# Kernel tuning notes

Hardware: AMD Instinct MI355X
Metric: run time of the kernel (lower is better)

## Reference

```python
import jax, jax.numpy as jnp
import numpy as np

N = 50000      # nodes
E = 800000     # edges (avg degree 16)
IN = 128       # in_dim0
H = 96         # hidden_dim
BN_EPS = 1e-5
PN_SCALE = 20.0


def setup_inputs() -> dict:
    key = jax.random.key(0)
    ks = jax.random.split(key, 12)
    s_in = 1.0 / np.sqrt(IN)
    s_h = 1.0 / np.sqrt(H)
    return {
        "x": jax.random.normal(ks[0], (N, IN), jnp.float32),
        "edge_index": jax.random.randint(ks[1], (2, E), 0, N, jnp.int32),
        # mlp0: Linear(in_dim0 -> hidden)
        "W0": jax.random.uniform(ks[2], (H, IN), jnp.float32, -s_in, s_in),
        "b0": jax.random.uniform(ks[3], (H,), jnp.float32, -s_in, s_in),
        # GIN MLP layer 1: Linear(hidden -> hidden) + BatchNorm
        "W1": jax.random.uniform(ks[4], (H, H), jnp.float32, -s_h, s_h),
        "b1": jax.random.uniform(ks[5], (H,), jnp.float32, -s_h, s_h),
        "gamma": jnp.ones((H,), jnp.float32),
        "beta": jnp.zeros((H,), jnp.float32),
        # GIN MLP layer 2: Linear(hidden -> hidden)
        "W2": jax.random.uniform(ks[6], (H, H), jnp.float32, -s_h, s_h),
        "b2": jax.random.uniform(ks[7], (H,), jnp.float32, -s_h, s_h),
    }


def reference(x, edge_index, W0, b0, W1, b1, gamma, beta, W2, b2):
    # h0 = mlp0(x)
    h0 = x @ W0.T + b0                                   # [N, H]

    # GINConv (eps=0): z_i = h0_i + sum_{j->i} h0_j
    src, dst = edge_index[0], edge_index[1]
    agg = jax.ops.segment_sum(h0[src], dst, num_segments=N)  # [N, H]
    z = h0 + agg

    # GIN MLP (layer_num=2): Linear -> BatchNorm(train) -> ReLU -> Linear
    h = z @ W1.T + b1
    mean = h.mean(axis=0)
    var = h.var(axis=0)                                  # biased, like torch BN
    h = (h - mean) * jax.lax.rsqrt(var + BN_EPS) * gamma + beta
    h = jax.nn.relu(h)
    l1 = h @ W2.T + b2                                   # [N, H]

    # PairNorm 'PN-SCS', scale=20
    col_mean = l1.mean(axis=0)
    rownorm = jnp.sqrt(1e-6 + jnp.sum(l1 * l1, axis=1, keepdims=True))
    l1 = PN_SCALE * l1 / rownorm - col_mean

    return (l1, h0)
```

## Files before the change

### kernel.cpp

```cpp
#include <hip/hip_runtime.h>

#define NN 50000
#define IN_DIM 128
#define HD 96
#define BN_EPS 1e-5f
#define PN_SCALE 20.0f
#define SCAN_NB 196

__device__ __forceinline__ float4 ld4(const float* p) { return *(const float4*)p; }
__device__ __forceinline__ float4 add4(float4 a, float4 b) {
    return make_float4(a.x + b.x, a.y + b.y, a.z + b.z, a.w + b.w);
}

__global__ void zero_kernel(float* stats, int* cnt) {
    int i = blockIdx.x * blockDim.x + threadIdx.x;
    if (i < 1024) stats[i] = 0.0f;
    int j = i - 1024;
    if (j >= 0 && j < NN) cnt[j] = 0;
}

template<int K, int MODE>
__global__ __launch_bounds__(256) void gemm_tiled(
    const float* A, const float* __restrict__ W, const float* __restrict__ bias,
    float* out, const float* __restrict__ scale, const float* __restrict__ shift,
    float* __restrict__ gsum, float* __restrict__ gsumsq,
    float* __restrict__ gcol, float* __restrict__ growss,
    const int* __restrict__ hist_dst, int* __restrict__ hist_cnt, int histE)
{
    constexpr int CK = 32;
    __shared__ float sh[64 * (CK + 1) + HD * (CK + 1)];
    float* As = sh;
    float* Ws = sh + 64 * (CK + 1);

    const int t  = threadIdx.x;

    if (MODE == 0) {
        int e0 = blockIdx.x * 1024 + t * 4;
#pragma unroll
        for (int i = 0; i < 4; ++i) {
            int e = e0 + i;
            if (e < histE) atomicAdd(&hist_cnt[hist_dst[e]], 1);
        }
    }

    const int tx = t & 15;
    const int ty = t >> 4;
    const int base = blockIdx.x * 64;

    float acc[4][6];
#pragma unroll
    for (int i = 0; i < 4; ++i)
#pragma unroll
        for (int j = 0; j < 6; ++j) acc[i][j] = 0.0f;

    for (int kc = 0; kc < K; kc += CK) {
#pragma unroll
        for (int it = 0; it < 2; ++it) {
            int q = t + it * 256;
            int r = q >> 3, c4 = q & 7;
            int row = base + r;
            float4 v = make_float4(0.f, 0.f, 0.f, 0.f);
            if (row < NN) v = ld4(A + (size_t)row * K + kc + c4 * 4);
            if (MODE == 2) {
                float4 sc = ld4(scale + kc + c4 * 4);
                float4 shf = ld4(shift + kc + c4 * 4);
                v.x = fmaxf(v.x * sc.x + shf.x, 0.f);
                v.y = fmaxf(v.y * sc.y + shf.y, 0.f);
                v.z = fmaxf(v.z * sc.z + shf.z, 0.f);
                v.w = fmaxf(v.w * sc.w + shf.w, 0.f);
            }
            float* d = As + r * (CK + 1) + c4 * 4;
            d[0] = v.x; d[1] = v.y; d[2] = v.z; d[3] = v.w;
        }
#pragma unroll
        for (int it = 0; it < 3; ++it) {
            int q = t + it * 256;
            int r = q >> 3, c4 = q & 7;
            float4 v = ld4(W + (size_t)r * K + kc + c4 * 4);
            float* d = Ws + r * (CK + 1) + c4 * 4;
            d[0] = v.x; d[1] = v.y; d[2] = v.z; d[3] = v.w;
        }
        __syncthreads();
#pragma unroll
        for (int kk = 0; kk < CK; ++kk) {
            float a[4], b[6];
#pragma unroll
            for (int i = 0; i < 4; ++i) a[i] = As[(ty * 4 + i) * (CK + 1) + kk];
#pragma unroll
            for (int j = 0; j < 6; ++j) b[j] = Ws[(tx * 6 + j) * (CK + 1) + kk];
#pragma unroll
            for (int i = 0; i < 4; ++i)
#pragma unroll
                for (int j = 0; j < 6; ++j) acc[i][j] += a[i] * b[j];
        }
        __syncthreads();
    }

    float cv[4][6];
#pragma unroll
    for (int j = 0; j < 6; ++j) {
        float bs = bias[tx * 6 + j];
#pragma unroll
        for (int i = 0; i < 4; ++i) cv[i][j] = acc[i][j] + bs;
    }
#pragma unroll
    for (int i = 0; i < 4; ++i) {
        int row = base + ty * 4 + i;
        if (row < NN) {
#pragma unroll
            for (int j = 0; j < 6; ++j)
                out[(size_t)row * HD + tx * 6 + j] = cv[i][j];
        }
    }

    if (MODE == 1) {
        float* rs_sum = sh;
        float* rs_sq  = sh + 1536;
        __syncthreads();
#pragma unroll
        for (int j = 0; j < 6; ++j) {
            float s = 0.f, q = 0.f;
#pragma unroll
            for (int i = 0; i < 4; ++i) {
                int row = base + ty * 4 + i;
                float v = (row < NN) ? cv[i][j] : 0.f;
                s += v; q += v * v;
            }
            rs_sum[ty * HD + tx * 6 + j] = s;
            rs_sq[ty * HD + tx * 6 + j]  = q;
        }
        __syncthreads();
        if (t < HD) {
            float S = 0.f, Q = 0.f;
#pragma unroll
            for (int r = 0; r < 16; ++r) { S += rs_sum[r * HD + t]; Q += rs_sq[r * HD + t]; }
            atomicAdd(&gsum[t], S);
            atomicAdd(&gsumsq[t], Q);
        }
    }

    if (MODE == 2) {
        float* rs_sum = sh;
        float* rr     = sh + 1536;
        __syncthreads();
#pragma unroll
        for (int j = 0; j < 6; ++j) {
            float s = 0.f;
#pragma unroll
            for (int i = 0; i < 4; ++i) {
                int row = base + ty * 4 + i;
                s += (row < NN) ? cv[i][j] : 0.f;
            }
            rs_sum[ty * HD + tx * 6 + j] = s;
        }
#pragma unroll
        for (int i = 0; i < 4; ++i) {
            float q = 0.f;
#pragma unroll
            for (int j = 0; j < 6; ++j) q += cv[i][j] * cv[i][j];
            rr[(ty * 4 + i) * 16 + tx] = q;
        }
        __syncthreads();
        if (t < HD) {
            float S = 0.f;
#pragma unroll
            for (int r = 0; r < 16; ++r) S += rs_sum[r * HD + t];
            atomicAdd(&gcol[t], S);
        }
        if (t < 64) {
            int row = base + t;
            if (row < NN) {
                float S = 0.f;
#pragma unroll
                for (int g = 0; g < 16; ++g) S += rr[t * 16 + g];
                growss[row] = S;
            }
        }
    }
}

__global__ __launch_bounds__(256) void scan_part1(const int* __restrict__ cnt,
                                                  int* __restrict__ bsum) {
    __shared__ int sh[256];
    int i = blockIdx.x * 256 + threadIdx.x;
    int t = threadIdx.x;
    sh[t] = (i < NN) ? cnt[i] : 0;
    __syncthreads();
    for (int off = 128; off > 0; off >>= 1) {
        if (t < off) sh[t] += sh[t + off];
        __syncthreads();
    }
    if (t == 0) bsum[blockIdx.x] = sh[0];
}

__global__ __launch_bounds__(256) void scan_part2(int* __restrict__ bsum) {
    __shared__ int sh[256];
    int t = threadIdx.x;
    int v = (t < SCAN_NB) ? bsum[t] : 0;
    sh[t] = v;
    __syncthreads();
    for (int off = 1; off < 256; off <<= 1) {
        int u = sh[t];
        if (t >= off) u += sh[t - off];
        __syncthreads();
        sh[t] = u;
        __syncthreads();
    }
    if (t < SCAN_NB) bsum[t] = sh[t] - v;
}

__global__ __launch_bounds__(256) void scan_part3(int* __restrict__ cnt,
                                                  const int* __restrict__ bsum,
                                                  int* __restrict__ rowptr) {
    __shared__ int sh[256];
    int i = blockIdx.x * 256 + threadIdx.x;
    int t = threadIdx.x;
    int v = (i < NN) ? cnt[i] : 0;
    sh[t] = v;
    __syncthreads();
    for (int off = 1; off < 256; off <<= 1) {
        int u = sh[t];
        if (t >= off) u += sh[t - off];
        __syncthreads();
        sh[t] = u;
        __syncthreads();
    }
    int excl = sh[t] - v + bsum[blockIdx.x];
    if (i < NN) { rowptr[i] = excl; cnt[i] = excl; }
    if (i == NN - 1) rowptr[NN] = excl + v;
}

__global__ __launch_bounds__(256) void fill_kernel(const int* __restrict__ ei,
                                                   int* __restrict__ cursor,
                                                   int* __restrict__ srcs, int E) {
    int t2 = blockIdx.x * 256 + threadIdx.x;
    int e0 = t2 * 2;
    int src[2], dst[2];
#pragma unroll
    for (int i = 0; i < 2; ++i) {
        int e = e0 + i;
        bool ok = e < E;
        dst[i] = ok ? ei[E + e] : -1;
        src[i] = ok ? ei[e] : 0;
    }
    for (int pass = 0; pass < 7; ++pass) {
#pragma unroll
        for (int i = 0; i < 2; ++i) {
            if (dst[i] >= 0 && (dst[i] >> 13) == pass) {
                int slot = atomicAdd(&cursor[dst[i]], 1);
                srcs[slot] = src[i];
            }
        }
    }
}

__global__ __launch_bounds__(192) void gather_kernel(
    const float* __restrict__ h0, const int* __restrict__ rowptr,
    const int* __restrict__ srcs, float* __restrict__ z)
{
    const int tid = threadIdx.x;
    const int rl  = tid / 24;
    const int c   = tid - rl * 24;
    const int row = blockIdx.x * 8 + rl;
    if (row >= NN) return;

    const int p0 = rowptr[row];
    const int p1 = rowptr[row + 1];

    float4 acc = ld4(h0 + (size_t)row * HD + c * 4);

    int p = p0;
    for (; p + 8 <= p1; p += 8) {
        int s0 = srcs[p + 0], s1 = srcs[p + 1], s2 = srcs[p + 2], s3 = srcs[p + 3];
        int s4 = srcs[p + 4], s5 = srcs[p + 5], s6 = srcs[p + 6], s7 = srcs[p + 7];
        float4 v0 = ld4(h0 + (size_t)s0 * HD + c * 4);
        float4 v1 = ld4(h0 + (size_t)s1 * HD + c * 4);
        float4 v2 = ld4(h0 + (size_t)s2 * HD + c * 4);
        float4 v3 = ld4(h0 + (size_t)s3 * HD + c * 4);
        float4 v4 = ld4(h0 + (size_t)s4 * HD + c * 4);
        float4 v5 = ld4(h0 + (size_t)s5 * HD + c * 4);
        float4 v6 = ld4(h0 + (size_t)s6 * HD + c * 4);
        float4 v7 = ld4(h0 + (size_t)s7 * HD + c * 4);
        acc = add4(acc, add4(add4(add4(v0, v1), add4(v2, v3)),
                             add4(add4(v4, v5), add4(v6, v7))));
    }
    for (; p + 4 <= p1; p += 4) {
        int s0 = srcs[p + 0], s1 = srcs[p + 1], s2 = srcs[p + 2], s3 = srcs[p + 3];
        float4 v0 = ld4(h0 + (size_t)s0 * HD + c * 4);
        float4 v1 = ld4(h0 + (size_t)s1 * HD + c * 4);
        float4 v2 = ld4(h0 + (size_t)s2 * HD + c * 4);
        float4 v3 = ld4(h0 + (size_t)s3 * HD + c * 4);
        acc = add4(acc, add4(add4(v0, v1), add4(v2, v3)));
    }
    for (; p < p1; ++p)
        acc = add4(acc, ld4(h0 + (size_t)srcs[p] * HD + c * 4));

    *(float4*)(z + (size_t)row * HD + c * 4) = acc;
}

__global__ void bn_finalize_kernel(const float* __restrict__ sum, const float* __restrict__ sumsq,
                                   const float* __restrict__ gamma, const float* __restrict__ beta,
                                   float* __restrict__ scale, float* __restrict__ shift)
{
    int f = threadIdx.x;
    if (f < HD) {
        float mean = sum[f] * (1.0f / NN);
        float var  = fmaxf(sumsq[f] * (1.0f / NN) - mean * mean, 0.0f);
        float rstd = rsqrtf(var + BN_EPS);
        float sc = rstd * gamma[f];
        scale[f] = sc;
        shift[f] = beta[f] - mean * sc;
    }
}

__global__ __launch_bounds__(256) void pn_kernel(float* l1, const float* __restrict__ colsum,
                                                 const float* __restrict__ rowss)
{
    int idx = blockIdx.x * 256 + threadIdx.x;
    if (idx >= NN * 24) return;
    int row = idx / 24;
    int q = idx - row * 24;
    float rs = rsqrtf(1e-6f + rowss[row]);
    float4 v = ld4(l1 + (size_t)idx * 4);
    float4 cm = ld4(colsum + q * 4);
    v.x = PN_SCALE * v.x * rs - cm.x * (1.0f / NN);
    v.y = PN_SCALE * v.y * rs - cm.y * (1.0f / NN);
    v.z = PN_SCALE * v.z * rs - cm.z * (1.0f / NN);
    v.w = PN_SCALE * v.w * rs - cm.w * (1.0f / NN);
    *(float4*)(l1 + (size_t)idx * 4) = v;
}

extern "C" void kernel_launch(void* const* d_in, const int* in_sizes, int n_in,
                              void* d_out, int out_size, void* d_ws, size_t ws_size,
                              hipStream_t stream) {
    const float* x     = (const float*)d_in[0];
    const int*   ei    = (const int*)d_in[1];
    const float* W0    = (const float*)d_in[2];
    const float* b0    = (const float*)d_in[3];
    const float* W1    = (const float*)d_in[4];
    const float* b1    = (const float*)d_in[5];
    const float* gamma = (const float*)d_in[6];
    const float* beta  = (const float*)d_in[7];
    const float* W2    = (const float*)d_in[8];
    const float* b2    = (const float*)d_in[9];

    float* out_l1 = (float*)d_out;
    float* out_h0 = out_l1 + (size_t)NN * HD;

    float* stats   = (float*)d_ws;
    float* s_sum   = stats;
    float* s_sumsq = stats + HD;
    float* s_col   = stats + 2 * HD;
    float* s_scale = stats + 288;
    float* s_shift = stats + 384;
    float* rowss = stats + 1024;
    int* cnt    = (int*)(rowss + NN);
    int* rowptr = cnt + NN;
    int* bsum   = rowptr + NN + 2;
    int* srcs   = bsum + 256;

    const int E = in_sizes[1] / 2;
    const int GB = (NN + 63) / 64;

    zero_kernel<<<(1024 + NN + 255) / 256, 256, 0, stream>>>(stats, cnt);
    gemm_tiled<IN_DIM, 0><<<GB, 256, 0, stream>>>(x, W0, b0, out_h0, nullptr, nullptr,
                                                  nullptr, nullptr, nullptr, nullptr,
                                                  ei + E, cnt, E);
    scan_part1<<<SCAN_NB, 256, 0, stream>>>(cnt, bsum);
    scan_part2<<<1, 256, 0, stream>>>(bsum);
    scan_part3<<<SCAN_NB, 256, 0, stream>>>(cnt, bsum, rowptr);
    fill_kernel<<<(E / 2 + 255) / 256, 256, 0, stream>>>(ei, cnt, srcs, E);
    gather_kernel<<<(NN + 7) / 8, 192, 0, stream>>>(out_h0, rowptr, srcs, out_l1);
    gemm_tiled<HD, 1><<<GB, 256, 0, stream>>>(out_l1, W1, b1, out_l1, nullptr, nullptr,
                                              s_sum, s_sumsq, nullptr, nullptr,
                                              nullptr, nullptr, 0);
    bn_finalize_kernel<<<1, 128, 0, stream>>>(s_sum, s_sumsq, gamma, beta, s_scale, s_shift);
    gemm_tiled<HD, 2><<<GB, 256, 0, stream>>>(out_l1, W2, b2, out_l1, s_scale, s_shift,
                                              nullptr, nullptr, s_col, rowss,
                                              nullptr, nullptr, 0);
    pn_kernel<<<(NN * 24 + 255) / 256, 256, 0, stream>>>(out_l1, s_col, rowss);
}
```

Baseline: 337.6 us.

## Restructure GEMM tiles: transposed smem, vectorized reads, register prefetch

Changes the per-thread tile from 4x6 to 2x12 and stores A and W transposed in shared memory with padding, so the inner loop uses float2/float4 LDS reads instead of scalar ones. Global loads for the next K chunk are prefetched into registers while the current chunk computes (software pipelining). Output stores and bias loads are vectorized, and the BN/PairNorm reductions are adapted to the new 32x8 thread layout. This aims to cut LDS instruction count and hide global latency, at the cost of more registers and transposed smem writes that may bank-conflict.

```diff
diff --git a/kernel.cpp b/kernel.cpp
--- a/kernel.cpp
+++ b/kernel.cpp
@@ -27,10 +27,12 @@
     float* __restrict__ gcol, float* __restrict__ growss,
     const int* __restrict__ hist_dst, int* __restrict__ hist_cnt, int histE)
 {
-    constexpr int CK = 32;
-    __shared__ float sh[64 * (CK + 1) + HD * (CK + 1)];
+    constexpr int CK  = 32;
+    constexpr int APD = 66;
+    constexpr int WPD = 100;
+    __shared__ float sh[32 * APD + 32 * WPD];
     float* As = sh;
-    float* Ws = sh + 64 * (CK + 1);
+    float* Ws = sh + 32 * APD;
 
     const int t  = threadIdx.x;
 
@@ -43,128 +45,197 @@
         }
     }
 
-    const int tx = t & 15;
-    const int ty = t >> 4;
+    const int ty = t >> 3;
+    const int tx = t & 7;
     const int base = blockIdx.x * 64;
 
-    float acc[4][6];
-#pragma unroll
-    for (int i = 0; i < 4; ++i)
-#pragma unroll
-        for (int j = 0; j < 6; ++j) acc[i][j] = 0.0f;
-
-    for (int kc = 0; kc < K; kc += CK) {
+    float acc[2][12];
+#pragma unroll
+    for (int i = 0; i < 2; ++i)
+#pragma unroll
+        for (int j = 0; j < 12; ++j) acc[i][j] = 0.0f;
+
+    float4 pa[2], pw[3];
+
+    auto load_stage = [&](int kc) {
 #pragma unroll
         for (int it = 0; it < 2; ++it) {
             int q = t + it * 256;
             int r = q >> 3, c4 = q & 7;
             int row = base + r;
-            float4 v = make_float4(0.f, 0.f, 0.f, 0.f);
-            if (row < NN) v = ld4(A + (size_t)row * K + kc + c4 * 4);
+            pa[it] = (row < NN) ? ld4(A + (size_t)row * K + kc + c4 * 4)
+                                : make_float4(0.f, 0.f, 0.f, 0.f);
+        }
+#pragma unroll
+        for (int it = 0; it < 3; ++it) {
+            int q = t + it * 256;
+            int r = q >> 3, c4 = q & 7;
+            pw[it] = ld4(W + (size_t)r * K + kc + c4 * 4);
+        }
+    };
+
+    auto write_stage = [&](int kc) {
+#pragma unroll
+        for (int it = 0; it < 2; ++it) {
+            int q = t + it * 256;
+            int r = q >> 3, c4 = q & 7;
+            float4 v = pa[it];
             if (MODE == 2) {
-                float4 sc = ld4(scale + kc + c4 * 4);
+                float4 sc  = ld4(scale + kc + c4 * 4);
                 float4 shf = ld4(shift + kc + c4 * 4);
                 v.x = fmaxf(v.x * sc.x + shf.x, 0.f);
                 v.y = fmaxf(v.y * sc.y + shf.y, 0.f);
                 v.z = fmaxf(v.z * sc.z + shf.z, 0.f);
                 v.w = fmaxf(v.w * sc.w + shf.w, 0.f);
             }
-            float* d = As + r * (CK + 1) + c4 * 4;
-            d[0] = v.x; d[1] = v.y; d[2] = v.z; d[3] = v.w;
+            As[(c4 * 4 + 0) * APD + r] = v.x;
+            As[(c4 * 4 + 1) * APD + r] = v.y;
+            As[(c4 * 4 + 2) * APD + r] = v.z;
+            As[(c4 * 4 + 3) * APD + r] = v.w;
         }
 #pragma unroll
         for (int it = 0; it < 3; ++it) {
             int q = t + it * 256;
             int r = q >> 3, c4 = q & 7;
-            float4 v = ld4(W + (size_t)r * K + kc + c4 * 4);
-            float* d = Ws + r * (CK + 1) + c4 * 4;
-            d[0] = v.x; d[1] = v.y; d[2] = v.z; d[3] = v.w;
-        }
-        __syncthreads();
-#pragma unroll
+            float4 v = pw[it];
+            Ws[(c4 * 4 + 0) * WPD + r] = v.x;
+            Ws[(c4 * 4 + 1) * WPD + r] = v.y;
+            Ws[(c4 * 4 + 2) * WPD + r] = v.z;
+            Ws[(c4 * 4 + 3) * WPD + r] = v.w;
+        }
+    };
+
+    load_stage(0);
+    for (int kc = 0; kc < K; kc += CK) {
+        write_stage(kc);
+        __syncthreads();
+        if (kc + CK < K) load_stage(kc + CK);
+#pragma unroll 8
         for (int kk = 0; kk < CK; ++kk) {
-            float a[4], b[6];
-#pragma unroll
-            for (int i = 0; i < 4; ++i) a[i] = As[(ty * 4 + i) * (CK + 1) + kk];
-#pragma unroll
-            for (int j = 0; j < 6; ++j) b[j] = Ws[(tx * 6 + j) * (CK + 1) + kk];
-#pragma unroll
-            for (int i = 0; i < 4; ++i)
-#pragma unroll
-                for (int j = 0; j < 6; ++j) acc[i][j] += a[i] * b[j];
-        }
-        __syncthreads();
-    }
-
-    float cv[4][6];
-#pragma unroll
-    for (int j = 0; j < 6; ++j) {
-        float bs = bias[tx * 6 + j];
-#pragma unroll
-        for (int i = 0; i < 4; ++i) cv[i][j] = acc[i][j] + bs;
-    }
-#pragma unroll
-    for (int i = 0; i < 4; ++i) {
-        int row = base + ty * 4 + i;
+            float2 a = *(const float2*)(As + kk * APD + ty * 2);
+            float4 w0 = ld4(Ws + kk * WPD + tx * 12);
+            float4 w1 = ld4(Ws + kk * WPD + tx * 12 + 4);
+            float4 w2 = ld4(Ws + kk * WPD + tx * 12 + 8);
+            float av[2] = {a.x, a.y};
+            float wv[12] = {w0.x, w0.y, w0.z, w0.w,
+                            w1.x, w1.y, w1.z, w1.w,
+                            w2.x, w2.y, w2.z, w2.w};
+#pragma unroll
+            for (int i = 0; i < 2; ++i)
+#pragma unroll
+                for (int j = 0; j < 12; ++j) acc[i][j] += av[i] * wv[j];
+        }
+        __syncthreads();
+    }
+
+    float cv[2][12];
+    float4 b0v = ld4(bias + tx * 12);
+    float4 b1v = ld4(bias + tx * 12 + 4);
+    float4 b2v = ld4(bias + tx * 12 + 8);
+    float bv[12] = {b0v.x, b0v.y, b0v.z, b0v.w,
+                    b1v.x, b1v.y, b1v.z, b1v.w,
+                    b2v.x, b2v.y, b2v.z, b2v.w};
+#pragma unroll
+    for (int i = 0; i < 2; ++i)
+#pragma unroll
+        for (int j = 0; j < 12; ++j) cv[i][j] = acc[i][j] + bv[j];
+
+#pragma unroll
+    for (int i = 0; i < 2; ++i) {
+        int row = base + ty * 2 + i;
         if (row < NN) {
-#pragma unroll
-            for (int j = 0; j < 6; ++j)
-                out[(size_t)row * HD + tx * 6 + j] = cv[i][j];
+            float* o = out + (size_t)row * HD + tx * 12;
+            *(float4*)(o + 0) = make_float4(cv[i][0], cv[i][1], cv[i][2],  cv[i][3]);
+            *(float4*)(o + 4) = make_float4(cv[i][4], cv[i][5], cv[i][6],  cv[i][7]);
+            *(float4*)(o + 8) = make_float4(cv[i][8], cv[i][9], cv[i][10], cv[i][11]);
         }
     }
 
     if (MODE == 1) {
-        float* rs_sum = sh;
-        float* rs_sq  = sh + 1536;
-        __syncthreads();
-#pragma unroll
-        for (int j = 0; j < 6; ++j) {
-            float s = 0.f, q = 0.f;
-#pragma unroll
-            for (int i = 0; i < 4; ++i) {
-                int row = base + ty * 4 + i;
-                float v = (row < NN) ? cv[i][j] : 0.f;
-                s += v; q += v * v;
-            }
-            rs_sum[ty * HD + tx * 6 + j] = s;
-            rs_sq[ty * HD + tx * 6 + j]  = q;
-        }
-        __syncthreads();
-        if (t < HD) {
-            float S = 0.f, Q = 0.f;
-#pragma unroll
-            for (int r = 0; r < 16; ++r) { S += rs_sum[r * HD + t]; Q += rs_sq[r * HD + t]; }
-            atomicAdd(&gsum[t], S);
-            atomicAdd(&gsumsq[t], Q);
-        }
-    }
-
-    if (MODE == 2) {
-        float* rs_sum = sh;
-        float* rr     = sh + 1536;
-        __syncthreads();
-#pragma unroll
-        for (int j = 0; j < 6; ++j) {
-            float s = 0.f;
-#pragma unroll
-            for (int i = 0; i < 4; ++i) {
-                int row = base + ty * 4 + i;
-                s += (row < NN) ? cv[i][j] : 0.f;
-            }
-            rs_sum[ty * HD + tx * 6 + j] = s;
-        }
-#pragma unroll
-        for (int i = 0; i < 4; ++i) {
-            float q = 0.f;
-#pragma unroll
-            for (int j = 0; j < 6; ++j) q += cv[i][j] * cv[i][j];
-            rr[(ty * 4 + i) * 16 + tx] = q;
+        float* rs = sh;
+        __syncthreads();
+        {
+            float s[12];
+#pragma unroll
+            for (int j = 0; j < 12; ++j) {
+                s[j] = 0.f;
+#pragma unroll
+                for (int i = 0; i < 2; ++i) {
+                    int row = base + ty * 2 + i;
+                    s[j] += (row < NN) ? cv[i][j] : 0.f;
+                }
+            }
+            float* d = rs + ty * HD + tx * 12;
+            *(float4*)(d + 0) = make_float4(s[0], s[1], s[2],  s[3]);
+            *(float4*)(d + 4) = make_float4(s[4], s[5], s[6],  s[7]);
+            *(float4*)(d + 8) = make_float4(s[8], s[9], s[10], s[11]);
         }
         __syncthreads();
         if (t < HD) {
             float S = 0.f;
 #pragma unroll
-            for (int r = 0; r < 16; ++r) S += rs_sum[r * HD + t];
+            for (int r = 0; r < 32; ++r) S += rs[r * HD + t];
+            atomicAdd(&gsum[t], S);
+        }
+        __syncthreads();
+        {
+            float s[12];
+#pragma unroll
+            for (int j = 0; j < 12; ++j) {
+                s[j] = 0.f;
+#pragma unroll
+                for (int i = 0; i < 2; ++i) {
+                    int row = base + ty * 2 + i;
+                    float v = (row < NN) ? cv[i][j] : 0.f;
+                    s[j] += v * v;
+                }
+            }
+            float* d = rs + ty * HD + tx * 12;
+            *(float4*)(d + 0) = make_float4(s[0], s[1], s[2],  s[3]);
+            *(float4*)(d + 4) = make_float4(s[4], s[5], s[6],  s[7]);
+            *(float4*)(d + 8) = make_float4(s[8], s[9], s[10], s[11]);
+        }
+        __syncthreads();
+        if (t < HD) {
+            float Q = 0.f;
+#pragma unroll
+            for (int r = 0; r < 32; ++r) Q += rs[r * HD + t];
+            atomicAdd(&gsumsq[t], Q);
+        }
+    }
+
+    if (MODE == 2) {
+        float* rs = sh;
+        float* rr = sh + 32 * HD;
+        __syncthreads();
+        {
+            float s[12];
+#pragma unroll
+            for (int j = 0; j < 12; ++j) {
+                s[j] = 0.f;
+#pragma unroll
+                for (int i = 0; i < 2; ++i) {
+                    int row = base + ty * 2 + i;
+                    s[j] += (row < NN) ? cv[i][j] : 0.f;
+                }
+            }
+            float* d = rs + ty * HD + tx * 12;
+            *(float4*)(d + 0) = make_float4(s[0], s[1], s[2],  s[3]);
+            *(float4*)(d + 4) = make_float4(s[4], s[5], s[6],  s[7]);
+            *(float4*)(d + 8) = make_float4(s[8], s[9], s[10], s[11]);
+#pragma unroll
+            for (int i = 0; i < 2; ++i) {
+                float q = 0.f;
+#pragma unroll
+                for (int j = 0; j < 12; ++j) q += cv[i][j] * cv[i][j];
+                rr[(ty * 2 + i) * 8 + tx] = q;
+            }
+        }
+        __syncthreads();
+        if (t < HD) {
+            float S = 0.f;
+#pragma unroll
+            for (int r = 0; r < 32; ++r) S += rs[r * HD + t];
             atomicAdd(&gcol[t], S);
         }
         if (t < 64) {
@@ -172,7 +243,7 @@
             if (row < NN) {
                 float S = 0.f;
 #pragma unroll
-                for (int g = 0; g < 16; ++g) S += rr[t * 16 + g];
+                for (int g = 0; g < 8; ++g) S += rr[t * 8 + g];
                 growss[row] = S;
             }
         }
```

Result: no change. 331.1 us (-1.9%).

## Replace LDS-tiled GEMMs with row-per-lane kernel using wave-uniform weight loads

Applied to the files above, without the earlier changes.

The three dense GEMMs no longer stage A and W tiles through shared memory. In the new kernel each lane owns one row, and each of 8 waves owns 12 output columns. Weight addresses are made wave-uniform with readfirstlane so they can be served as broadcast or scalar loads, and A is prefetched one 16-wide chunk ahead into registers. The BN column statistics now use wave shuffle reductions instead of shared-memory reductions, and the histogram step loads int2. The risks are strided per-lane loads of A that are not coalesced, and each row being re-read by 8 waves, which leans on cache hits.

```diff
diff --git a/kernel.cpp b/kernel.cpp
--- a/kernel.cpp
+++ b/kernel.cpp
@@ -20,161 +20,141 @@
 }
 
 template<int K, int MODE>
-__global__ __launch_bounds__(256) void gemm_tiled(
-    const float* A, const float* __restrict__ W, const float* __restrict__ bias,
-    float* out, const float* __restrict__ scale, const float* __restrict__ shift,
+__global__ __launch_bounds__(512) void gemm_sw(
+    const float* __restrict__ A, const float* __restrict__ W, const float* __restrict__ bias,
+    float* __restrict__ out, const float* __restrict__ scale, const float* __restrict__ shift,
     float* __restrict__ gsum, float* __restrict__ gsumsq,
     float* __restrict__ gcol, float* __restrict__ growss,
-    const int* __restrict__ hist_dst, int* __restrict__ hist_cnt, int histE)
+    const int* __restrict__ ei, int* __restrict__ hist_cnt, int E)
 {
-    constexpr int CK = 32;
-    __shared__ float sh[64 * (CK + 1) + HD * (CK + 1)];
-    float* As = sh;
-    float* Ws = sh + 64 * (CK + 1);
-
-    const int t  = threadIdx.x;
+    __shared__ float rss[8][64];
+    const int tid  = threadIdx.x;
+    const int lane = tid & 63;
+    const int wid  = tid >> 6;
+    const int cb   = __builtin_amdgcn_readfirstlane(wid * 12);
+    const int row  = blockIdx.x * 64 + lane;
+    const bool rok = row < NN;
 
     if (MODE == 0) {
-        int e0 = blockIdx.x * 1024 + t * 4;
-#pragma unroll
-        for (int i = 0; i < 4; ++i) {
-            int e = e0 + i;
-            if (e < histE) atomicAdd(&hist_cnt[hist_dst[e]], 1);
-        }
-    }
-
-    const int tx = t & 15;
-    const int ty = t >> 4;
-    const int base = blockIdx.x * 64;
-
-    float acc[4][6];
-#pragma unroll
-    for (int i = 0; i < 4; ++i)
-#pragma unroll
-        for (int j = 0; j < 6; ++j) acc[i][j] = 0.0f;
-
-    for (int kc = 0; kc < K; kc += CK) {
-#pragma unroll
-        for (int it = 0; it < 2; ++it) {
-            int q = t + it * 256;
-            int r = q >> 3, c4 = q & 7;
-            int row = base + r;
-            float4 v = make_float4(0.f, 0.f, 0.f, 0.f);
-            if (row < NN) v = ld4(A + (size_t)row * K + kc + c4 * 4);
+        int e0 = (blockIdx.x * 512 + tid) * 2;
+        if (e0 + 2 <= E) {
+            int2 d2 = *(const int2*)(ei + E + e0);
+            atomicAdd(&hist_cnt[d2.x], 1);
+            atomicAdd(&hist_cnt[d2.y], 1);
+        } else if (e0 < E) {
+            atomicAdd(&hist_cnt[ei[E + e0]], 1);
+        }
+    }
+
+    const float* Wp = W + (size_t)cb * K;
+    const float* Ap = A + (size_t)row * K;
+
+    float acc[12];
+#pragma unroll
+    for (int j = 0; j < 12; ++j) acc[j] = 0.f;
+
+    constexpr int NB = K / 16;
+    float4 pa[4], pb[4];
+#pragma unroll
+    for (int u = 0; u < 4; ++u)
+        pa[u] = rok ? ld4(Ap + u * 4) : make_float4(0.f, 0.f, 0.f, 0.f);
+
+#pragma unroll
+    for (int b = 0; b < NB; ++b) {
+        if (b + 1 < NB) {
+#pragma unroll
+            for (int u = 0; u < 4; ++u)
+                pb[u] = rok ? ld4(Ap + (b + 1) * 16 + u * 4)
+                            : make_float4(0.f, 0.f, 0.f, 0.f);
+        }
+#pragma unroll
+        for (int u = 0; u < 4; ++u) {
+            const int kc = b * 16 + u * 4;
+            float av[4];
             if (MODE == 2) {
-                float4 sc = ld4(scale + kc + c4 * 4);
-                float4 shf = ld4(shift + kc + c4 * 4);
-                v.x = fmaxf(v.x * sc.x + shf.x, 0.f);
-                v.y = fmaxf(v.y * sc.y + shf.y, 0.f);
-                v.z = fmaxf(v.z * sc.z + shf.z, 0.f);
-                v.w = fmaxf(v.w * sc.w + shf.w, 0.f);
-            }
-            float* d = As + r * (CK + 1) + c4 * 4;
-            d[0] = v.x; d[1] = v.y; d[2] = v.z; d[3] = v.w;
-        }
-#pragma unroll
-        for (int it = 0; it < 3; ++it) {
-            int q = t + it * 256;
-            int r = q >> 3, c4 = q & 7;
-            float4 v = ld4(W + (size_t)r * K + kc + c4 * 4);
-            float* d = Ws + r * (CK + 1) + c4 * 4;
-            d[0] = v.x; d[1] = v.y; d[2] = v.z; d[3] = v.w;
-        }
-        __syncthreads();
-#pragma unroll
-        for (int kk = 0; kk < CK; ++kk) {
-            float a[4], b[6];
-#pragma unroll
-            for (int i = 0; i < 4; ++i) a[i] = As[(ty * 4 + i) * (CK + 1) + kk];
-#pragma unroll
-            for (int j = 0; j < 6; ++j) b[j] = Ws[(tx * 6 + j) * (CK + 1) + kk];
-#pragma unroll
-            for (int i = 0; i < 4; ++i)
-#pragma unroll
-                for (int j = 0; j < 6; ++j) acc[i][j] += a[i] * b[j];
-        }
-        __syncthreads();
-    }
-
-    float cv[4][6];
-#pragma unroll
-    for (int j = 0; j < 6; ++j) {
-        float bs = bias[tx * 6 + j];
-#pragma unroll
-        for (int i = 0; i < 4; ++i) cv[i][j] = acc[i][j] + bs;
-    }
-#pragma unroll
-    for (int i = 0; i < 4; ++i) {
-        int row = base + ty * 4 + i;
-        if (row < NN) {
-#pragma unroll
-            for (int j = 0; j < 6; ++j)
-                out[(size_t)row * HD + tx * 6 + j] = cv[i][j];
-        }
+                float4 sc = ld4(scale + kc), sh = ld4(shift + kc);
+                av[0] = fmaxf(pa[u].x * sc.x + sh.x, 0.f);
+                av[1] = fmaxf(pa[u].y * sc.y + sh.y, 0.f);
+                av[2] = fmaxf(pa[u].z * sc.z + sh.z, 0.f);
+                av[3] = fmaxf(pa[u].w * sc.w + sh.w, 0.f);
+            } else {
+                av[0] = pa[u].x; av[1] = pa[u].y; av[2] = pa[u].z; av[3] = pa[u].w;
+            }
+#pragma unroll
+            for (int j = 0; j < 12; ++j) {
+                float4 w4 = ld4(Wp + j * K + kc);
+                acc[j] = fmaf(av[0], w4.x, acc[j]);
+                acc[j] = fmaf(av[1], w4.y, acc[j]);
+                acc[j] = fmaf(av[2], w4.z, acc[j]);
+                acc[j] = fmaf(av[3], w4.w, acc[j]);
+            }
+        }
+#pragma unroll
+        for (int u = 0; u < 4; ++u) pa[u] = pb[u];
+    }
+
+    if (MODE != 0) __syncthreads();
+
+    float cv[12];
+    {
+        float4 b0 = ld4(bias + cb), b1 = ld4(bias + cb + 4), b2 = ld4(bias + cb + 8);
+        float bv[12] = {b0.x, b0.y, b0.z, b0.w, b1.x, b1.y, b1.z, b1.w,
+                        b2.x, b2.y, b2.z, b2.w};
+#pragma unroll
+        for (int j = 0; j < 12; ++j) cv[j] = acc[j] + bv[j];
+    }
+    if (rok) {
+        float* o = out + (size_t)row * HD + cb;
+        *(float4*)(o + 0) = make_float4(cv[0], cv[1], cv[2],  cv[3]);
+        *(float4*)(o + 4) = make_float4(cv[4], cv[5], cv[6],  cv[7]);
+        *(float4*)(o + 8) = make_float4(cv[8], cv[9], cv[10], cv[11]);
     }
 
     if (MODE == 1) {
-        float* rs_sum = sh;
-        float* rs_sq  = sh + 1536;
-        __syncthreads();
-#pragma unroll
-        for (int j = 0; j < 6; ++j) {
-            float s = 0.f, q = 0.f;
-#pragma unroll
-            for (int i = 0; i < 4; ++i) {
-                int row = base + ty * 4 + i;
-                float v = (row < NN) ? cv[i][j] : 0.f;
-                s += v; q += v * v;
-            }
-            rs_sum[ty * HD + tx * 6 + j] = s;
-            rs_sq[ty * HD + tx * 6 + j]  = q;
-        }
-        __syncthreads();
-        if (t < HD) {
-            float S = 0.f, Q = 0.f;
-#pragma unroll
-            for (int r = 0; r < 16; ++r) { S += rs_sum[r * HD + t]; Q += rs_sq[r * HD + t]; }
-            atomicAdd(&gsum[t], S);
-            atomicAdd(&gsumsq[t], Q);
+        float s[12], q[12];
+#pragma unroll
+        for (int j = 0; j < 12; ++j) {
+            float v = rok ? cv[j] : 0.f;
+            s[j] = v; q[j] = v * v;
+        }
+#pragma unroll
+        for (int d = 1; d <= 32; d <<= 1)
+#pragma unroll
+            for (int j = 0; j < 12; ++j) {
+                s[j] += __shfl_xor(s[j], d);
+                q[j] += __shfl_xor(q[j], d);
+            }
+        if (lane == 0) {
+#pragma unroll
+            for (int j = 0; j < 12; ++j) {
+                atomicAdd(&gsum[cb + j], s[j]);
+                atomicAdd(&gsumsq[cb + j], q[j]);
+            }
         }
     }
 
     if (MODE == 2) {
-        float* rs_sum = sh;
-        float* rr     = sh + 1536;
-        __syncthreads();
-#pragma unroll
-        for (int j = 0; j < 6; ++j) {
-            float s = 0.f;
-#pragma unroll
-            for (int i = 0; i < 4; ++i) {
-                int row = base + ty * 4 + i;
-                s += (row < NN) ? cv[i][j] : 0.f;
-            }
-            rs_sum[ty * HD + tx * 6 + j] = s;
-        }
-#pragma unroll
-        for (int i = 0; i < 4; ++i) {
-            float q = 0.f;
-#pragma unroll
-            for (int j = 0; j < 6; ++j) q += cv[i][j] * cv[i][j];
-            rr[(ty * 4 + i) * 16 + tx] = q;
-        }
-        __syncthreads();
-        if (t < HD) {
+        float s[12];
+#pragma unroll
+        for (int j = 0; j < 12; ++j) s[j] = rok ? cv[j] : 0.f;
+#pragma unroll
+        for (int d = 1; d <= 32; d <<= 1)
+#pragma unroll
+            for (int j = 0; j < 12; ++j) s[j] += __shfl_xor(s[j], d);
+        if (lane == 0) {
+#pragma unroll
+            for (int j = 0; j < 12; ++j) atomicAdd(&gcol[cb + j], s[j]);
+        }
+        float rq = 0.f;
+#pragma unroll
+        for (int j = 0; j < 12; ++j) rq = fmaf(cv[j], cv[j], rq);
+        rss[wid][lane] = rq;
+        __syncthreads();
+        if (wid == 0 && rok) {
             float S = 0.f;
 #pragma unroll
-            for (int r = 0; r < 16; ++r) S += rs_sum[r * HD + t];
-            atomicAdd(&gcol[t], S);
-        }
-        if (t < 64) {
-            int row = base + t;
-            if (row < NN) {
-                float S = 0.f;
-#pragma unroll
-                for (int g = 0; g < 16; ++g) S += rr[t * 16 + g];
-                growss[row] = S;
-            }
+            for (int g = 0; g < 8; ++g) S += rss[g][lane];
+            growss[row] = S;
         }
     }
 }
@@ -363,20 +343,20 @@
     const int GB = (NN + 63) / 64;
 
     zero_kernel<<<(1024 + NN + 255) / 256, 256, 0, stream>>>(stats, cnt);
-    gemm_tiled<IN_DIM, 0><<<GB, 256, 0, stream>>>(x, W0, b0, out_h0, nullptr, nullptr,
-                                                  nullptr, nullptr, nullptr, nullptr,
-                                                  ei + E, cnt, E);
+    gemm_sw<IN_DIM, 0><<<GB, 512, 0, stream>>>(x, W0, b0, out_h0, nullptr, nullptr,
+                                               nullptr, nullptr, nullptr, nullptr,
+                                               ei, cnt, E);
     scan_part1<<<SCAN_NB, 256, 0, stream>>>(cnt, bsum);
     scan_part2<<<1, 256, 0, stream>>>(bsum);
     scan_part3<<<SCAN_NB, 256, 0, stream>>>(cnt, bsum, rowptr);
     fill_kernel<<<(E / 2 + 255) / 256, 256, 0, stream>>>(ei, cnt, srcs, E);
     gather_kernel<<<(NN + 7) / 8, 192, 0, stream>>>(out_h0, rowptr, srcs, out_l1);
-    gemm_tiled<HD, 1><<<GB, 256, 0, stream>>>(out_l1, W1, b1, out_l1, nullptr, nullptr,
-                                              s_sum, s_sumsq, nullptr, nullptr,
-                                              nullptr, nullptr, 0);
+    gemm_sw<HD, 1><<<GB, 512, 0, stream>>>(out_l1, W1, b1, out_l1, nullptr, nullptr,
+                                           s_sum, s_sumsq, nullptr, nullptr,
+                                           nullptr, nullptr, 0);
     bn_finalize_kernel<<<1, 128, 0, stream>>>(s_sum, s_sumsq, gamma, beta, s_scale, s_shift);
-    gemm_tiled<HD, 2><<<GB, 256, 0, stream>>>(out_l1, W2, b2, out_l1, s_scale, s_shift,
-                                              nullptr, nullptr, s_col, rowss,
-                                              nullptr, nullptr, 0);
+    gemm_sw<HD, 2><<<GB, 512, 0, stream>>>(out_l1, W2, b2, out_l1, s_scale, s_shift,
+                                           nullptr, nullptr, s_col, rowss,
+                                           nullptr, nullptr, 0);
     pn_kernel<<<(NN * 24 + 255) / 256, 256, 0, stream>>>(out_l1, s_col, rowss);
 }
```

Result: slower. 940.5 us (+178.6%).

## Retile GEMM to 4x12 per thread with transposed smem and register prefetch

Applied to the files above, without the earlier changes.

The shared GEMM kernel moves from 256 to 128 threads per block, and each thread now computes a 4x12 output tile instead of 4x6. The A and W tiles are stored k-major in shared memory, so the inner loop reads them with float4 loads. The next K-chunk is prefetched into registers while the current one is computed, and the output stores and the edge-histogram loads are vectorised. The goal is more FMA work per shared-memory access and hidden global load latency, at the cost of more registers per thread and fewer threads per block.

```diff
diff --git a/kernel.cpp b/kernel.cpp
--- a/kernel.cpp
+++ b/kernel.cpp
@@ -20,114 +20,162 @@
 }
 
 template<int K, int MODE>
-__global__ __launch_bounds__(256) void gemm_tiled(
+__global__ __launch_bounds__(128) void gemm_tiled(
     const float* A, const float* __restrict__ W, const float* __restrict__ bias,
     float* out, const float* __restrict__ scale, const float* __restrict__ shift,
     float* __restrict__ gsum, float* __restrict__ gsumsq,
     float* __restrict__ gcol, float* __restrict__ growss,
-    const int* __restrict__ hist_dst, int* __restrict__ hist_cnt, int histE)
+    const int* __restrict__ ei, int* __restrict__ hist_cnt, int E)
 {
-    constexpr int CK = 32;
-    __shared__ float sh[64 * (CK + 1) + HD * (CK + 1)];
+    constexpr int CK  = 32;
+    constexpr int APD = 68;
+    constexpr int WPD = 100;
+    __shared__ float sh[CK * APD + CK * WPD];
     float* As = sh;
-    float* Ws = sh + 64 * (CK + 1);
+    float* Ws = sh + CK * APD;
 
     const int t  = threadIdx.x;
+    const int tx = t & 7;
+    const int ty = t >> 3;
+    const int base = blockIdx.x * 64;
 
     if (MODE == 0) {
-        int e0 = blockIdx.x * 1024 + t * 4;
-#pragma unroll
-        for (int i = 0; i < 4; ++i) {
-            int e = e0 + i;
-            if (e < histE) atomicAdd(&hist_cnt[hist_dst[e]], 1);
-        }
-    }
-
-    const int tx = t & 15;
-    const int ty = t >> 4;
-    const int base = blockIdx.x * 64;
-
-    float acc[4][6];
+        int e0 = (blockIdx.x * 128 + t) * 8;
+        if (e0 + 8 <= E) {
+            int4 a4 = *(const int4*)(ei + E + e0);
+            int4 b4 = *(const int4*)(ei + E + e0 + 4);
+            atomicAdd(&hist_cnt[a4.x], 1); atomicAdd(&hist_cnt[a4.y], 1);
+            atomicAdd(&hist_cnt[a4.z], 1); atomicAdd(&hist_cnt[a4.w], 1);
+            atomicAdd(&hist_cnt[b4.x], 1); atomicAdd(&hist_cnt[b4.y], 1);
+            atomicAdd(&hist_cnt[b4.z], 1); atomicAdd(&hist_cnt[b4.w], 1);
+        } else {
+            for (int i = 0; i < 8; ++i) {
+                int e = e0 + i;
+                if (e < E) atomicAdd(&hist_cnt[ei[E + e]], 1);
+            }
+        }
+    }
+
+    float acc[4][12];
 #pragma unroll
     for (int i = 0; i < 4; ++i)
 #pragma unroll
-        for (int j = 0; j < 6; ++j) acc[i][j] = 0.0f;
-
-    for (int kc = 0; kc < K; kc += CK) {
-#pragma unroll
-        for (int it = 0; it < 2; ++it) {
-            int q = t + it * 256;
+        for (int j = 0; j < 12; ++j) acc[i][j] = 0.0f;
+
+    float4 pa[4], pw[6];
+
+    auto load_stage = [&](int kc) {
+#pragma unroll
+        for (int it = 0; it < 4; ++it) {
+            int q = t + it * 128;
             int r = q >> 3, c4 = q & 7;
             int row = base + r;
-            float4 v = make_float4(0.f, 0.f, 0.f, 0.f);
-            if (row < NN) v = ld4(A + (size_t)row * K + kc + c4 * 4);
+            pa[it] = (row < NN) ? ld4(A + (size_t)row * K + kc + c4 * 4)
+                                : make_float4(0.f, 0.f, 0.f, 0.f);
+        }
+#pragma unroll
+        for (int it = 0; it < 6; ++it) {
+            int q = t + it * 128;
+            int col = q >> 3, c4 = q & 7;
+            pw[it] = ld4(W + (size_t)col * K + kc + c4 * 4);
+        }
+    };
+
+    auto write_stage = [&](int kc) {
+#pragma unroll
+        for (int it = 0; it < 4; ++it) {
+            int q = t + it * 128;
+            int r = q >> 3, c4 = q & 7;
+            float4 v = pa[it];
             if (MODE == 2) {
-                float4 sc = ld4(scale + kc + c4 * 4);
+                float4 sc  = ld4(scale + kc + c4 * 4);
                 float4 shf = ld4(shift + kc + c4 * 4);
                 v.x = fmaxf(v.x * sc.x + shf.x, 0.f);
                 v.y = fmaxf(v.y * sc.y + shf.y, 0.f);
                 v.z = fmaxf(v.z * sc.z + shf.z, 0.f);
                 v.w = fmaxf(v.w * sc.w + shf.w, 0.f);
             }
-            float* d = As + r * (CK + 1) + c4 * 4;
-            d[0] = v.x; d[1] = v.y; d[2] = v.z; d[3] = v.w;
-        }
-#pragma unroll
-        for (int it = 0; it < 3; ++it) {
-            int q = t + it * 256;
-            int r = q >> 3, c4 = q & 7;
-            float4 v = ld4(W + (size_t)r * K + kc + c4 * 4);
-            float* d = Ws + r * (CK + 1) + c4 * 4;
-            d[0] = v.x; d[1] = v.y; d[2] = v.z; d[3] = v.w;
-        }
-        __syncthreads();
-#pragma unroll
+            As[(c4 * 4 + 0) * APD + r] = v.x;
+            As[(c4 * 4 + 1) * APD + r] = v.y;
+            As[(c4 * 4 + 2) * APD + r] = v.z;
+            As[(c4 * 4 + 3) * APD + r] = v.w;
+        }
+#pragma unroll
+        for (int it = 0; it < 6; ++it) {
+            int q = t + it * 128;
+            int col = q >> 3, c4 = q & 7;
+            float4 v = pw[it];
+            Ws[(c4 * 4 + 0) * WPD + col] = v.x;
+            Ws[(c4 * 4 + 1) * WPD + col] = v.y;
+            Ws[(c4 * 4 + 2) * WPD + col] = v.z;
+            Ws[(c4 * 4 + 3) * WPD + col] = v.w;
+        }
+    };
+
+    load_stage(0);
+    for (int kc = 0; kc < K; kc += CK) {
+        write_stage(kc);
+        __syncthreads();
+        if (kc + CK < K) load_stage(kc + CK);
+#pragma unroll 8
         for (int kk = 0; kk < CK; ++kk) {
-            float a[4], b[6];
-#pragma unroll
-            for (int i = 0; i < 4; ++i) a[i] = As[(ty * 4 + i) * (CK + 1) + kk];
-#pragma unroll
-            for (int j = 0; j < 6; ++j) b[j] = Ws[(tx * 6 + j) * (CK + 1) + kk];
+            float4 a  = ld4(As + kk * APD + ty * 4);
+            float4 w0 = ld4(Ws + kk * WPD + tx * 12);
+            float4 w1 = ld4(Ws + kk * WPD + tx * 12 + 4);
+            float4 w2 = ld4(Ws + kk * WPD + tx * 12 + 8);
+            float av[4] = {a.x, a.y, a.z, a.w};
+            float wv[12] = {w0.x, w0.y, w0.z, w0.w,
+                            w1.x, w1.y, w1.z, w1.w,
+                            w2.x, w2.y, w2.z, w2.w};
 #pragma unroll
             for (int i = 0; i < 4; ++i)
 #pragma unroll
-                for (int j = 0; j < 6; ++j) acc[i][j] += a[i] * b[j];
-        }
-        __syncthreads();
-    }
-
-    float cv[4][6];
-#pragma unroll
-    for (int j = 0; j < 6; ++j) {
-        float bs = bias[tx * 6 + j];
-#pragma unroll
-        for (int i = 0; i < 4; ++i) cv[i][j] = acc[i][j] + bs;
+                for (int j = 0; j < 12; ++j)
+                    acc[i][j] = fmaf(av[i], wv[j], acc[i][j]);
+        }
+        __syncthreads();
+    }
+
+    float cv[4][12];
+    {
+        float4 b0 = ld4(bias + tx * 12), b1 = ld4(bias + tx * 12 + 4),
+               b2 = ld4(bias + tx * 12 + 8);
+        float bv[12] = {b0.x, b0.y, b0.z, b0.w, b1.x, b1.y, b1.z, b1.w,
+                        b2.x, b2.y, b2.z, b2.w};
+#pragma unroll
+        for (int i = 0; i < 4; ++i)
+#pragma unroll
+            for (int j = 0; j < 12; ++j) cv[i][j] = acc[i][j] + bv[j];
     }
 #pragma unroll
     for (int i = 0; i < 4; ++i) {
         int row = base + ty * 4 + i;
         if (row < NN) {
-#pragma unroll
-            for (int j = 0; j < 6; ++j)
-                out[(size_t)row * HD + tx * 6 + j] = cv[i][j];
+            float* o = out + (size_t)row * HD + tx * 12;
+            *(float4*)(o + 0) = make_float4(cv[i][0], cv[i][1], cv[i][2],  cv[i][3]);
+            *(float4*)(o + 4) = make_float4(cv[i][4], cv[i][5], cv[i][6],  cv[i][7]);
+            *(float4*)(o + 8) = make_float4(cv[i][8], cv[i][9], cv[i][10], cv[i][11]);
         }
     }
 
     if (MODE == 1) {
         float* rs_sum = sh;
         float* rs_sq  = sh + 1536;
-        __syncthreads();
-#pragma unroll
-        for (int j = 0; j < 6; ++j) {
-            float s = 0.f, q = 0.f;
+        float s[12], q[12];
+#pragma unroll
+        for (int j = 0; j < 12; ++j) {
+            s[j] = 0.f; q[j] = 0.f;
 #pragma unroll
             for (int i = 0; i < 4; ++i) {
                 int row = base + ty * 4 + i;
                 float v = (row < NN) ? cv[i][j] : 0.f;
-                s += v; q += v * v;
-            }
-            rs_sum[ty * HD + tx * 6 + j] = s;
-            rs_sq[ty * HD + tx * 6 + j]  = q;
+                s[j] += v; q[j] += v * v;
+            }
+        }
+#pragma unroll
+        for (int j = 0; j < 12; ++j) {
+            rs_sum[ty * HD + tx * 12 + j] = s[j];
+            rs_sq[ty * HD + tx * 12 + j]  = q[j];
         }
         __syncthreads();
         if (t < HD) {
@@ -142,23 +190,25 @@
     if (MODE == 2) {
         float* rs_sum = sh;
         float* rr     = sh + 1536;
-        __syncthreads();
-#pragma unroll
-        for (int j = 0; j < 6; ++j) {
-            float s = 0.f;
+        float s[12];
+#pragma unroll
+        for (int j = 0; j < 12; ++j) {
+            s[j] = 0.f;
 #pragma unroll
             for (int i = 0; i < 4; ++i) {
                 int row = base + ty * 4 + i;
-                s += (row < NN) ? cv[i][j] : 0.f;
-            }
-            rs_sum[ty * HD + tx * 6 + j] = s;
-        }
+                s[j] += (row < NN) ? cv[i][j] : 0.f;
+            }
+        }
+#pragma unroll
+        for (int j = 0; j < 12; ++j)
+            rs_sum[ty * HD + tx * 12 + j] = s[j];
 #pragma unroll
         for (int i = 0; i < 4; ++i) {
             float q = 0.f;
 #pragma unroll
-            for (int j = 0; j < 6; ++j) q += cv[i][j] * cv[i][j];
-            rr[(ty * 4 + i) * 16 + tx] = q;
+            for (int j = 0; j < 12; ++j) q = fmaf(cv[i][j], cv[i][j], q);
+            rr[(ty * 4 + i) * 8 + tx] = q;
         }
         __syncthreads();
         if (t < HD) {
@@ -172,7 +222,7 @@
             if (row < NN) {
                 float S = 0.f;
 #pragma unroll
-                for (int g = 0; g < 16; ++g) S += rr[t * 16 + g];
+                for (int g = 0; g < 8; ++g) S += rr[t * 8 + g];
                 growss[row] = S;
             }
         }
@@ -363,19 +413,19 @@
     const int GB = (NN + 63) / 64;
 
     zero_kernel<<<(1024 + NN + 255) / 256, 256, 0, stream>>>(stats, cnt);
-    gemm_tiled<IN_DIM, 0><<<GB, 256, 0, stream>>>(x, W0, b0, out_h0, nullptr, nullptr,
+    gemm_tiled<IN_DIM, 0><<<GB, 128, 0, stream>>>(x, W0, b0, out_h0, nullptr, nullptr,
                                                   nullptr, nullptr, nullptr, nullptr,
-                                                  ei + E, cnt, E);
+                                                  ei, cnt, E);
     scan_part1<<<SCAN_NB, 256, 0, stream>>>(cnt, bsum);
     scan_part2<<<1, 256, 0, stream>>>(bsum);
     scan_part3<<<SCAN_NB, 256, 0, stream>>>(cnt, bsum, rowptr);
     fill_kernel<<<(E / 2 + 255) / 256, 256, 0, stream>>>(ei, cnt, srcs, E);
     gather_kernel<<<(NN + 7) / 8, 192, 0, stream>>>(out_h0, rowptr, srcs, out_l1);
-    gemm_tiled<HD, 1><<<GB, 256, 0, stream>>>(out_l1, W1, b1, out_l1, nullptr, nullptr,
+    gemm_tiled<HD, 1><<<GB, 128, 0, stream>>>(out_l1, W1, b1, out_l1, nullptr, nullptr,
                                               s_sum, s_sumsq, nullptr, nullptr,
                                               nullptr, nullptr, 0);
     bn_finalize_kernel<<<1, 128, 0, stream>>>(s_sum, s_sumsq, gamma, beta, s_scale, s_shift);
-    gemm_tiled<HD, 2><<<GB, 256, 0, stream>>>(out_l1, W2, b2, out_l1, s_scale, s_shift,
+    gemm_tiled<HD, 2><<<GB, 128, 0, stream>>>(out_l1, W2, b2, out_l1, s_scale, s_shift,
                                               nullptr, nullptr, s_col, rowss,
                                               nullptr, nullptr, 0);
     pn_kernel<<<(NN * 24 + 255) / 256, 256, 0, stream>>>(out_l1, s_col, rowss);
```

Result: faster. 329.6 us (-2.4%).
